# Kernel tuning notes

Hardware: AMD Instinct MI355X
Metric: run time of the kernel (lower is better)

## Reference

```python
import jax, jax.numpy as jnp
import numpy as np

NEG_INF = -1e6  # d2l masked_softmax fill value


def setup_inputs() -> dict:
    key = jax.random.key(0)
    kq, kk, kv, kl = jax.random.split(key, 4)
    n, s, d = 32, 2048, 64
    queries = jax.random.normal(kq, (n, s, d), dtype=jnp.float32)
    keys = jax.random.normal(kk, (n, s, d), dtype=jnp.float32)
    values = jax.random.normal(kv, (n, s, d), dtype=jnp.float32)
    valid_lens = jax.random.randint(kl, (n,), 1, s + 1, dtype=jnp.int32)
    return {"queries": queries, "keys": keys, "values": values, "valid_lens": valid_lens}


def reference(queries, keys, values, valid_lens):
    d = queries.shape[-1]
    # scores: [n, q, k]
    scores = jnp.einsum("nqd,nkd->nqk", queries, keys) / jnp.sqrt(jnp.float32(d))
    kv_len = scores.shape[-1]
    # masked_softmax: positions >= valid_len get NEG_INF before softmax
    mask = jnp.arange(kv_len, dtype=jnp.int32)[None, None, :] < valid_lens[:, None, None]
    scores = jnp.where(mask, scores, NEG_INF)
    attn = jax.nn.softmax(scores, axis=-1)
    # dropout rate 0.0 (inference) -> identity
    return jnp.einsum("nqk,nkd->nqd", attn, values)
```

## Files before the change

kernel.cpp:

```cpp
#include <hip/hip_runtime.h>
#include <hip/hip_bf16.h>


typedef short bf16x8 __attribute__((ext_vector_type(8)));
typedef float f32x4  __attribute__((ext_vector_type(4)));
typedef unsigned int u32;
typedef u32 u32x2 __attribute__((ext_vector_type(2)));
typedef u32 u32x4 __attribute__((ext_vector_type(4)));

#define SEQ 2048
#define DH 64
#define BK 64
#define LDSP 72
#define CPAD 68
#define SCLQ 0.18033688011112042f

static __device__ __forceinline__ short f2bf(float f) {
    unsigned u = __float_as_uint(f);
    return (short)((u + 0x7FFFu + ((u >> 16) & 1u)) >> 16);
}
static __device__ __forceinline__ u32 pk2bf(float lo, float hi) {
    __hip_bfloat162 h = __float22bfloat162_rn(float2{lo, hi});
    return *(u32*)&h;
}

__global__ __launch_bounds__(256, 4)
void prepass(const float* __restrict__ K, const float* __restrict__ V,
             short* __restrict__ Kp, short* __restrict__ Vp)
{
    __shared__ short T[DH][LDSP];

    const int tid  = threadIdx.x;
    const int wave = tid >> 6;
    const int lane = tid & 63;
    const int b  = blockIdx.x & 31;
    const int kt = blockIdx.x >> 5;
    const int k0 = kt * BK;
    const size_t bo = (size_t)b * SEQ * DH;
    const size_t tb = (size_t)(b * 32 + kt) * 4096;

    #pragma unroll
    for (int h = 0; h < 2; ++h) {
        const int o   = tid + h * 256;
        const int f   = o >> 6;
        const int ln  = o & 63;
        const int l15 = ln >> 2;
        const int g   = ln & 3;
        const float* src = K + bo + (size_t)(k0 + (f >> 1) * 16 + l15) * DH
                         + (f & 1) * 32 + g * 8;
        f32x4 a = *(const f32x4*)(src);
        f32x4 c = *(const f32x4*)(src + 4);
        u32x4 w;
        w[0] = pk2bf(a[0], a[1]); w[1] = pk2bf(a[2], a[3]);
        w[2] = pk2bf(c[0], c[1]); w[3] = pk2bf(c[2], c[3]);
        *(u32x4*)(Kp + tb + (size_t)o * 8) = w;
    }

    #pragma unroll
    for (int h = 0; h < 2; ++h) {
        const int d0 = wave * 8 + h * 32;
        const float* src = V + bo + (size_t)(k0 + lane) * DH + d0;
        f32x4 va = *(const f32x4*)(src);
        f32x4 vb = *(const f32x4*)(src + 4);
        #pragma unroll
        for (int j = 0; j < 4; ++j) {
            T[d0 + j][lane]     = f2bf(va[j]);
            T[d0 + 4 + j][lane] = f2bf(vb[j]);
        }
    }
    __syncthreads();

    #pragma unroll
    for (int h = 0; h < 2; ++h) {
        const int o   = tid + h * 256;
        const int f   = o >> 6;
        const int ln  = o & 63;
        const int l15 = ln >> 2;
        const int g   = ln & 3;
        const int db  = f >> 1;
        const int cc  = f & 1;
        bf16x8 v = *(const bf16x8*)(&T[db * 16 + l15][cc * 32 + g * 8]);
        *(bf16x8*)(Vp + tb + (size_t)o * 8) = v;
    }
}

__global__ __launch_bounds__(256, 2)
void attn_fwd(const float* __restrict__ Q,
              const short* __restrict__ Kp, const short* __restrict__ Vp,
              const int* __restrict__ VL, float* __restrict__ O)
{
    __shared__ float Comb[4][64][CPAD];
    __shared__ float CombL[4][64];
    __shared__ short Pw[4][16][LDSP];
    __shared__ int   Rsort[32];

    const int tid  = threadIdx.x;
    const int wave = tid >> 6;
    const int lane = tid & 63;
    const int g    = lane >> 4;
    const int l15  = lane & 15;

    if (tid < 32) {
        const int nv = (VL[tid] + BK - 1) >> 6;
        int rank = 0;
        for (int jj = 0; jj < 32; ++jj) {
            const int nj = (VL[jj] + BK - 1) >> 6;
            rank += (nj > nv) || (nj == nv && jj < tid);
        }
        Rsort[rank] = tid;
    }
    __syncthreads();

    const int rank = blockIdx.x >> 5;
    const int qt   = blockIdx.x & 31;
    const int b    = Rsort[rank];

    const int vl  = VL[b];
    const int nkt = (vl + BK - 1) >> 6;

    const size_t bo = (size_t)b * SEQ * DH;
    const int loff = (l15 * 4 + g) * 8;
    const short* KpB = Kp + (size_t)b * 32 * 4096 + loff;
    const short* VpB = Vp + (size_t)b * 32 * 4096 + loff;

    bf16x8 aq[4][2];
    #pragma unroll
    for (int qb = 0; qb < 4; ++qb) {
        const float* qp = Q + bo + (size_t)(qt * 64 + qb * 16 + l15) * DH + g * 8;
        f32x4 q0 = *(const f32x4*)(qp);
        f32x4 q1 = *(const f32x4*)(qp + 4);
        f32x4 q2 = *(const f32x4*)(qp + 32);
        f32x4 q3 = *(const f32x4*)(qp + 36);
        #pragma unroll
        for (int j = 0; j < 4; ++j) {
            aq[qb][0][j]     = f2bf(q0[j] * SCLQ);
            aq[qb][0][j + 4] = f2bf(q1[j] * SCLQ);
            aq[qb][1][j]     = f2bf(q2[j] * SCLQ);
            aq[qb][1][j + 4] = f2bf(q3[j] * SCLQ);
        }
    }

    bf16x8 ones;
    #pragma unroll
    for (int j = 0; j < 8; ++j) ones[j] = (short)0x3F80;

    f32x4 oacc[4][4];
    #pragma unroll
    for (int i = 0; i < 4; ++i)
        #pragma unroll
        for (int j = 0; j < 4; ++j) oacc[i][j] = f32x4{0.f, 0.f, 0.f, 0.f};
    f32x4 lacc[4];
    #pragma unroll
    for (int i = 0; i < 4; ++i) lacc[i] = f32x4{0.f, 0.f, 0.f, 0.f};

    for (int kt = wave; kt < nkt; kt += 4) {
        const int k0 = kt * BK;
        const short* kp = KpB + (size_t)kt * 4096;
        const short* vp = VpB + (size_t)kt * 4096;

        bf16x8 kf[8], vf[8];
        #pragma unroll
        for (int f = 0; f < 8; ++f) kf[f] = *(const bf16x8*)(kp + f * 512);
        #pragma unroll
        for (int f = 0; f < 8; ++f) vf[f] = *(const bf16x8*)(vp + f * 512);

        const bool full = (k0 + BK <= vl);

        #pragma unroll
        for (int qb = 0; qb < 4; ++qb) {
            f32x4 s[4];
            #pragma unroll
            for (int nb = 0; nb < 4; ++nb) {
                f32x4 acc = f32x4{0.f, 0.f, 0.f, 0.f};
                acc = __builtin_amdgcn_mfma_f32_16x16x32_bf16(kf[nb * 2 + 0], aq[qb][0], acc, 0, 0, 0);
                acc = __builtin_amdgcn_mfma_f32_16x16x32_bf16(kf[nb * 2 + 1], aq[qb][1], acc, 0, 0, 0);
                s[nb] = acc;
            }

            if (full) {
                #pragma unroll
                for (int nb = 0; nb < 4; ++nb)
                    #pragma unroll
                    for (int r = 0; r < 4; ++r)
                        s[nb][r] = __builtin_amdgcn_exp2f(s[nb][r]);
            } else {
                #pragma unroll
                for (int nb = 0; nb < 4; ++nb)
                    #pragma unroll
                    for (int r = 0; r < 4; ++r) {
                        const bool ok = (k0 + nb * 16 + g * 4 + r) < vl;
                        s[nb][r] = ok ? __builtin_amdgcn_exp2f(s[nb][r]) : 0.f;
                    }
            }

            #pragma unroll
            for (int nb = 0; nb < 4; ++nb) {
                u32x2 pkv;
                pkv[0] = pk2bf(s[nb][0], s[nb][1]);
                pkv[1] = pk2bf(s[nb][2], s[nb][3]);
                *(u32x2*)(&Pw[wave][l15][nb * 16 + g * 4]) = pkv;
            }
            asm volatile("" ::: "memory");

            #pragma unroll
            for (int cc = 0; cc < 2; ++cc) {
                bf16x8 ap = *(const bf16x8*)(&Pw[wave][l15][cc * 32 + g * 8]);
                lacc[qb] = __builtin_amdgcn_mfma_f32_16x16x32_bf16(ap, ones, lacc[qb], 0, 0, 0);
                #pragma unroll
                for (int db = 0; db < 4; ++db)
                    oacc[qb][db] = __builtin_amdgcn_mfma_f32_16x16x32_bf16(ap, vf[db * 2 + cc], oacc[qb][db], 0, 0, 0);
            }
            asm volatile("" ::: "memory");
        }
    }

    #pragma unroll
    for (int qb = 0; qb < 4; ++qb)
        #pragma unroll
        for (int db = 0; db < 4; ++db)
            #pragma unroll
            for (int r = 0; r < 4; ++r)
                Comb[wave][qb * 16 + g * 4 + r][db * 16 + l15] = oacc[qb][db][r];
    if (l15 == 0) {
        #pragma unroll
        for (int qb = 0; qb < 4; ++qb)
            #pragma unroll
            for (int r = 0; r < 4; ++r)
                CombL[wave][qb * 16 + g * 4 + r] = lacc[qb][r];
    }
    __syncthreads();

    const int q  = tid >> 2;
    const int d0 = (tid & 3) * 16;
    const float lsum = CombL[0][q] + CombL[1][q] + CombL[2][q] + CombL[3][q];
    const float inv = 1.0f / lsum;
    float* outp = O + bo + (size_t)(qt * 64 + q) * DH + d0;
    #pragma unroll
    for (int j = 0; j < 4; ++j) {
        f32x4 a0 = *(const f32x4*)(&Comb[0][q][d0 + 4 * j]);
        f32x4 a1 = *(const f32x4*)(&Comb[1][q][d0 + 4 * j]);
        f32x4 a2 = *(const f32x4*)(&Comb[2][q][d0 + 4 * j]);
        f32x4 a3 = *(const f32x4*)(&Comb[3][q][d0 + 4 * j]);
        f32x4 rsl = (a0 + a1 + a2 + a3) * inv;
        *(f32x4*)(outp + 4 * j) = rsl;
    }
}

__global__ __launch_bounds__(256, 4)
void attn_fwd_fb(const float* __restrict__ Q, const float* __restrict__ Kf,
                 const float* __restrict__ Vf, const int* __restrict__ VL,
                 float* __restrict__ O)
{
    __shared__ short Klds[BK][LDSP];
    __shared__ short Vt[DH][LDSP];
    __shared__ short Pw[4][16][LDSP];

    const int tid  = threadIdx.x;
    const int wave = tid >> 6;
    const int lane = tid & 63;
    const int g    = lane >> 4;
    const int l15  = lane & 15;
    const int b  = blockIdx.x & 31;
    const int qt = blockIdx.x >> 5;
    const int vl  = VL[b];
    const int nkt = (vl + BK - 1) >> 6;
    const size_t bo = (size_t)b * SEQ * DH;

    const int qrow = qt * 64 + wave * 16 + l15;
    bf16x8 aq0, aq1;
    {
        const float* qp = Q + bo + (size_t)qrow * DH + g * 8;
        f32x4 q0 = *(const f32x4*)(qp);
        f32x4 q1 = *(const f32x4*)(qp + 4);
        f32x4 q2 = *(const f32x4*)(qp + 32);
        f32x4 q3 = *(const f32x4*)(qp + 36);
        #pragma unroll
        for (int j = 0; j < 4; ++j) {
            aq0[j] = f2bf(q0[j] * SCLQ); aq0[j + 4] = f2bf(q1[j] * SCLQ);
            aq1[j] = f2bf(q2[j] * SCLQ); aq1[j + 4] = f2bf(q3[j] * SCLQ);
        }
    }
    bf16x8 ones;
    #pragma unroll
    for (int j = 0; j < 8; ++j) ones[j] = (short)0x3F80;
    f32x4 oacc[4];
    #pragma unroll
    for (int i = 0; i < 4; ++i) oacc[i] = f32x4{0.f, 0.f, 0.f, 0.f};
    f32x4 lacc = f32x4{0.f, 0.f, 0.f, 0.f};

    for (int kt = 0; kt < nkt; ++kt) {
        const int k0 = kt * BK;
        #pragma unroll
        for (int h = 0; h < 4; ++h) {
            const int cc = tid + h * 256;
            f32x4 v = *(const f32x4*)(Kf + bo + (size_t)(k0 + (cc >> 4)) * DH + (cc & 15) * 4);
            u32x2 o; o[0] = pk2bf(v[0], v[1]); o[1] = pk2bf(v[2], v[3]);
            *(u32x2*)(&Klds[cc >> 4][(cc & 15) * 4]) = o;
        }
        #pragma unroll
        for (int h = 0; h < 2; ++h) {
            const int d0 = wave * 8 + h * 32;
            const float* src = Vf + bo + (size_t)(k0 + lane) * DH + d0;
            f32x4 va = *(const f32x4*)(src);
            f32x4 vb = *(const f32x4*)(src + 4);
            #pragma unroll
            for (int j = 0; j < 4; ++j) {
                Vt[d0 + j][lane] = f2bf(va[j]); Vt[d0 + 4 + j][lane] = f2bf(vb[j]);
            }
        }
        __syncthreads();

        f32x4 s[4];
        #pragma unroll
        for (int nb = 0; nb < 4; ++nb) {
            bf16x8 ak0 = *(const bf16x8*)(&Klds[nb * 16 + l15][g * 8]);
            bf16x8 ak1 = *(const bf16x8*)(&Klds[nb * 16 + l15][32 + g * 8]);
            f32x4 acc = f32x4{0.f, 0.f, 0.f, 0.f};
            acc = __builtin_amdgcn_mfma_f32_16x16x32_bf16(ak0, aq0, acc, 0, 0, 0);
            acc = __builtin_amdgcn_mfma_f32_16x16x32_bf16(ak1, aq1, acc, 0, 0, 0);
            s[nb] = acc;
        }
        #pragma unroll
        for (int nb = 0; nb < 4; ++nb)
            #pragma unroll
            for (int r = 0; r < 4; ++r) {
                const bool ok = (k0 + nb * 16 + g * 4 + r) < vl;
                s[nb][r] = ok ? __builtin_amdgcn_exp2f(s[nb][r]) : 0.f;
            }
        #pragma unroll
        for (int nb = 0; nb < 4; ++nb) {
            u32x2 pkv;
            pkv[0] = pk2bf(s[nb][0], s[nb][1]);
            pkv[1] = pk2bf(s[nb][2], s[nb][3]);
            *(u32x2*)(&Pw[wave][l15][nb * 16 + g * 4]) = pkv;
        }
        asm volatile("" ::: "memory");
        #pragma unroll
        for (int cc = 0; cc < 2; ++cc) {
            bf16x8 ap = *(const bf16x8*)(&Pw[wave][l15][cc * 32 + g * 8]);
            lacc = __builtin_amdgcn_mfma_f32_16x16x32_bf16(ap, ones, lacc, 0, 0, 0);
            #pragma unroll
            for (int db = 0; db < 4; ++db) {
                bf16x8 bv = *(const bf16x8*)(&Vt[db * 16 + l15][cc * 32 + g * 8]);
                oacc[db] = __builtin_amdgcn_mfma_f32_16x16x32_bf16(ap, bv, oacc[db], 0, 0, 0);
            }
        }
        __syncthreads();
    }
    #pragma unroll
    for (int r = 0; r < 4; ++r) {
        const float inv = 1.0f / lacc[r];
        const int row = qt * 64 + wave * 16 + g * 4 + r;
        #pragma unroll
        for (int db = 0; db < 4; ++db)
            O[bo + (size_t)row * DH + db * 16 + l15] = oacc[db][r] * inv;
    }
}

extern "C" void kernel_launch(void* const* d_in, const int* in_sizes, int n_in,
                              void* d_out, int out_size, void* d_ws, size_t ws_size,
                              hipStream_t stream) {
    const float* Q  = (const float*)d_in[0];
    const float* K  = (const float*)d_in[1];
    const float* V  = (const float*)d_in[2];
    const int*   VL = (const int*)d_in[3];
    float* O = (float*)d_out;

    const size_t nel = (size_t)32 * SEQ * DH;
    const size_t need = 2 * nel * sizeof(short);
    if (ws_size >= need) {
        short* Kp = (short*)d_ws;
        short* Vp = Kp + nel;
        prepass<<<dim3(1024), dim3(256), 0, stream>>>(K, V, Kp, Vp);
        attn_fwd<<<dim3(1024), dim3(256), 0, stream>>>(Q, Kp, Vp, VL, O);
    } else {
        attn_fwd_fb<<<dim3(1024), dim3(256), 0, stream>>>(Q, K, V, VL, O);
    }
}
```

Baseline: 128.6 us.

## Shrink combine LDS buffer to raise occupancy and balance batch-to-block ordering

The cross-wave combine buffer shrinks from 64 rows to 16 and is reused in four passes, one per query block, with barriers between passes. This cuts LDS use per block so the launch bound can go from 2 to 4 blocks per CU. Block-to-batch assignment is also changed to interleave long and short valid-length batches in a serpentine order, so concurrently resident blocks carry mixed work. The costs are extra synchronizations in the epilogue and a tighter register budget under the higher launch bound, which could cause spilling.

```diff
diff --git a/kernel.cpp b/kernel.cpp
--- a/kernel.cpp
+++ b/kernel.cpp
@@ -84,13 +84,13 @@
     }
 }
 
-__global__ __launch_bounds__(256, 2)
+__global__ __launch_bounds__(256, 4)
 void attn_fwd(const float* __restrict__ Q,
               const short* __restrict__ Kp, const short* __restrict__ Vp,
               const int* __restrict__ VL, float* __restrict__ O)
 {
-    __shared__ float Comb[4][64][CPAD];
-    __shared__ float CombL[4][64];
+    __shared__ float CombO[4][16][CPAD];
+    __shared__ float CombL[4][16];
     __shared__ short Pw[4][16][LDSP];
     __shared__ int   Rsort[32];
 
@@ -111,9 +111,13 @@
     }
     __syncthreads();
 
-    const int rank = blockIdx.x >> 5;
-    const int qt   = blockIdx.x & 31;
-    const int b    = Rsort[rank];
+    const int jb = blockIdx.x & 255;
+    const int sl = blockIdx.x >> 8;
+    const int c8 = jb >> 5;
+    const int qt = jb & 31;
+    const int rk = (sl == 0) ? c8 : (sl == 1) ? (15 - c8)
+                 : (sl == 2) ? (16 + c8) : (31 - c8);
+    const int b  = Rsort[rk];
 
     const int vl  = VL[b];
     const int nkt = (vl + BK - 1) >> 6;
@@ -214,35 +218,31 @@
         }
     }
 
-    #pragma unroll
-    for (int qb = 0; qb < 4; ++qb)
+    const int q16 = tid >> 4;
+    const int d0  = (tid & 15) * 4;
+    #pragma unroll
+    for (int qb = 0; qb < 4; ++qb) {
         #pragma unroll
         for (int db = 0; db < 4; ++db)
             #pragma unroll
             for (int r = 0; r < 4; ++r)
-                Comb[wave][qb * 16 + g * 4 + r][db * 16 + l15] = oacc[qb][db][r];
-    if (l15 == 0) {
-        #pragma unroll
-        for (int qb = 0; qb < 4; ++qb)
+                CombO[wave][g * 4 + r][db * 16 + l15] = oacc[qb][db][r];
+        if (l15 == 0) {
             #pragma unroll
             for (int r = 0; r < 4; ++r)
-                CombL[wave][qb * 16 + g * 4 + r] = lacc[qb][r];
-    }
-    __syncthreads();
-
-    const int q  = tid >> 2;
-    const int d0 = (tid & 3) * 16;
-    const float lsum = CombL[0][q] + CombL[1][q] + CombL[2][q] + CombL[3][q];
-    const float inv = 1.0f / lsum;
-    float* outp = O + bo + (size_t)(qt * 64 + q) * DH + d0;
-    #pragma unroll
-    for (int j = 0; j < 4; ++j) {
-        f32x4 a0 = *(const f32x4*)(&Comb[0][q][d0 + 4 * j]);
-        f32x4 a1 = *(const f32x4*)(&Comb[1][q][d0 + 4 * j]);
-        f32x4 a2 = *(const f32x4*)(&Comb[2][q][d0 + 4 * j]);
-        f32x4 a3 = *(const f32x4*)(&Comb[3][q][d0 + 4 * j]);
-        f32x4 rsl = (a0 + a1 + a2 + a3) * inv;
-        *(f32x4*)(outp + 4 * j) = rsl;
+                CombL[wave][g * 4 + r] = lacc[qb][r];
+        }
+        __syncthreads();
+
+        const float lsum = CombL[0][q16] + CombL[1][q16] + CombL[2][q16] + CombL[3][q16];
+        const float inv = 1.0f / lsum;
+        f32x4 a = *(const f32x4*)(&CombO[0][q16][d0]);
+        a = a + *(const f32x4*)(&CombO[1][q16][d0]);
+        a = a + *(const f32x4*)(&CombO[2][q16][d0]);
+        a = a + *(const f32x4*)(&CombO[3][q16][d0]);
+        a = a * inv;
+        *(f32x4*)(O + bo + (size_t)(qt * 64 + qb * 16 + q16) * DH + d0) = a;
+        __syncthreads();
     }
 }
 
```

Result: slower. 262.3 us (+104.0%).
